# Performance work log

Hardware: AMD Instinct MI355X
Metric: run time of the kernel (lower is better)

The kernel has to match this reference:

```python
import jax, jax.numpy as jnp
import numpy as np

GAMMA = 0.5
K = 3
SKIP_THRESHOLD = 1.0


def setup_inputs() -> dict:
    key = jax.random.key(0)
    ks = jax.random.split(key, 11)
    in_dim, out_dim, mem_len = 1024, 128, 131072
    inp = {
        "x": jax.random.normal(ks[0], (1, in_dim), jnp.float32),
        "mean": jax.random.normal(ks[1], (in_dim,), jnp.float32),
        "std": jax.random.uniform(ks[2], (in_dim,), jnp.float32, 0.5, 1.5),
        "memory": jax.random.normal(ks[3], (mem_len, out_dim), jnp.float32),
        "mem_data": jax.random.normal(ks[4], (mem_len, in_dim), jnp.float32),
        "W_enc": jax.random.normal(ks[5], (in_dim, out_dim), jnp.float32) * 0.02,
        "b_enc": jnp.zeros((out_dim,), jnp.float32),
        "W_dec": jax.random.normal(ks[6], (out_dim, in_dim), jnp.float32) * 0.02,
        "b_dec": jnp.zeros((in_dim,), jnp.float32),
        "win_mean": jnp.zeros((), jnp.float32),   # WindowLoss running mean
        "win_std": jnp.ones((), jnp.float32),     # WindowLoss sample std (1 if population_std==0)
    }
    return inp


def reference(x, mean, std, memory, mem_data, W_enc, b_enc, W_dec, b_dec, win_mean, win_std):
    # normalize: new = (x - mean) / std, zero where std == 0
    new = jnp.where(std == 0, 0.0, (x - mean) / std)            # [1, in_dim]
    # encoder: Linear + Tanh
    enc = jnp.tanh(new @ W_enc + b_enc)                          # [1, out_dim]
    # window_loss: decoder reconstruction MSE, gated by ndtr of z-scored loss
    rec = enc @ W_dec + b_dec                                    # [1, in_dim]
    mse = jnp.mean((rec - new) ** 2)                             # scalar
    prob = jax.scipy.special.ndtr((mse - win_mean) / win_std)    # torch uses loss.item() -> constant
    win_loss = (SKIP_THRESHOLD - prob) / SKIP_THRESHOLD * mse
    # L1-distance top-k (smallest) against the memory bank
    dist = jnp.sum(jnp.abs(memory - enc), axis=1)                # [mem_len]
    neg_d, idx = jax.lax.top_k(-dist, K)
    distances = -neg_d                                           # [K] smallest distances
    expw = GAMMA ** jnp.arange(K, dtype=jnp.float32)
    loss_values = jnp.sum(distances * expw) / jnp.sum(expw)
    # conditional FIFO scatter update at the nearest index
    cond = loss_values <= win_loss
    i0 = idx[0]
    new_memory = jnp.where(cond, memory.at[i0].set(enc[0]), memory)
    new_mem_data = jnp.where(cond, mem_data.at[i0].set(x[0]), mem_data)
    loss_combined = win_loss + loss_values
    return loss_combined, new_memory, new_mem_data
```

## Files before the change

kernel.cpp:

```cpp
#include <hip/hip_runtime.h>
#include <math.h>
#include <float.h>

#define IN_DIM   1024
#define OUT_DIM  128
#define MEM_LEN  131072
#define COPY_GRID 1024
#define DIST_BLOCKS 2048

#define NA_FLOATS  ((long long)MEM_LEN * OUT_DIM)
#define NB_FLOATS  ((long long)MEM_LEN * IN_DIM)
#define N_TOTAL    (NA_FLOATS + NB_FLOATS)
#define NFRAMES    (N_TOTAL / 1024)
#define NPAIRS     (NFRAMES / 2)
#define FRAME_MEM  16384

typedef float f4 __attribute__((ext_vector_type(4)));

__device__ __forceinline__ void ins3(float v, int i,
    float& v0, int& i0, float& v1, int& i1, float& v2, int& i2) {
  if (v < v0 || (v == v0 && i < i0)) {
    v2 = v1; i2 = i1; v1 = v0; i1 = i0; v0 = v; i0 = i;
  } else if (v < v1 || (v == v1 && i < i1)) {
    v2 = v1; i2 = i1; v1 = v; i1 = i;
  } else if (v < v2 || (v == v2 && i < i2)) {
    v2 = v; i2 = i;
  }
}

__global__ __launch_bounds__(256) void k1a_enc(
    const float* __restrict__ x, const float* __restrict__ mean,
    const float* __restrict__ stdv, const float* __restrict__ W_enc,
    const float* __restrict__ b_enc, float* __restrict__ ws_enc) {
  const int o = blockIdx.x;
  const int t = threadIdx.x;
  float partial = 0.0f;
  #pragma unroll
  for (int j = 0; j < 4; ++j) {
    const int k = t + 256 * j;
    const float sd = stdv[k];
    const float nv = (sd == 0.0f) ? 0.0f : (x[k] - mean[k]) / sd;
    partial += nv * W_enc[k * OUT_DIM + o];
  }
  for (int off = 32; off; off >>= 1) partial += __shfl_xor(partial, off, 64);
  __shared__ float s[4];
  if ((t & 63) == 0) s[t >> 6] = partial;
  __syncthreads();
  if (t == 0) ws_enc[o] = tanhf(s[0] + s[1] + s[2] + s[3] + b_enc[o]);
}

__global__ __launch_bounds__(128) void k1b_dec(
    const float* __restrict__ x, const float* __restrict__ mean,
    const float* __restrict__ stdv, const float* __restrict__ W_dec,
    const float* __restrict__ b_dec, const float* __restrict__ ws_enc,
    float* __restrict__ ws_sse) {
  const int t = threadIdx.x;
  const int o = blockIdx.x * 128 + t;
  __shared__ float s_enc[OUT_DIM];
  s_enc[t] = ws_enc[t];
  __syncthreads();
  float r = b_dec[o];
  #pragma unroll 8
  for (int k = 0; k < OUT_DIM; ++k) r += s_enc[k] * W_dec[k * IN_DIM + o];
  const float sd = stdv[o];
  const float nv = (sd == 0.0f) ? 0.0f : (x[o] - mean[o]) / sd;
  const float diff = r - nv;
  float sq = diff * diff;
  for (int off = 32; off; off >>= 1) sq += __shfl_xor(sq, off, 64);
  __shared__ float sr[2];
  if ((t & 63) == 0) sr[t >> 6] = sq;
  __syncthreads();
  if (t == 0) ws_sse[blockIdx.x] = sr[0] + sr[1];
}

__global__ __launch_bounds__(256) void k2_dist(
    const float* __restrict__ memory, const float* __restrict__ ws_enc,
    float* __restrict__ topv, int* __restrict__ topi) {
  const int t = threadIdx.x;
  const int lane = t & 63;
  const int wid = t >> 6;
  const int half = lane >> 5;
  const int col  = lane & 31;
  const float4 e = reinterpret_cast<const float4*>(ws_enc)[col];
  const float4* m4 = reinterpret_cast<const float4*>(memory);
  float v0 = FLT_MAX, v1 = FLT_MAX, v2 = FLT_MAX;
  int i0 = 0x7fffffff, i1 = 0x7fffffff, i2 = 0x7fffffff;
  const int r0 = (blockIdx.x * 4 + wid) * 16;
  for (int rr = 0; rr < 16; rr += 2) {
    const float4 m = m4[(size_t)(r0 + rr) * 32 + lane];
    float d = fabsf(m.x - e.x) + fabsf(m.y - e.y)
            + fabsf(m.z - e.z) + fabsf(m.w - e.w);
    d += __shfl_xor(d, 1, 64);
    d += __shfl_xor(d, 2, 64);
    d += __shfl_xor(d, 4, 64);
    d += __shfl_xor(d, 8, 64);
    d += __shfl_xor(d, 16, 64);
    ins3(d, r0 + rr + half, v0, i0, v1, i1, v2, i2);
  }
  {
    const float w0 = __shfl_xor(v0, 32, 64);
    const float w1 = __shfl_xor(v1, 32, 64);
    const float w2 = __shfl_xor(v2, 32, 64);
    const int j0 = __shfl_xor(i0, 32, 64);
    const int j1 = __shfl_xor(i1, 32, 64);
    const int j2 = __shfl_xor(i2, 32, 64);
    ins3(w0, j0, v0, i0, v1, i1, v2, i2);
    ins3(w1, j1, v0, i0, v1, i1, v2, i2);
    ins3(w2, j2, v0, i0, v1, i1, v2, i2);
  }
  __shared__ float sv[4][3];
  __shared__ int   si[4][3];
  if (lane == 0) {
    sv[wid][0] = v0; sv[wid][1] = v1; sv[wid][2] = v2;
    si[wid][0] = i0; si[wid][1] = i1; si[wid][2] = i2;
  }
  __syncthreads();
  if (t == 0) {
    for (int w = 1; w < 4; ++w)
      for (int j = 0; j < 3; ++j)
        ins3(sv[w][j], si[w][j], v0, i0, v1, i1, v2, i2);
    topv[blockIdx.x * 3 + 0] = v0; topi[blockIdx.x * 3 + 0] = i0;
    topv[blockIdx.x * 3 + 1] = v1; topi[blockIdx.x * 3 + 1] = i1;
    topv[blockIdx.x * 3 + 2] = v2; topi[blockIdx.x * 3 + 2] = i2;
  }
}

__global__ __launch_bounds__(256) void copy_all(
    const float* __restrict__ memory, const float* __restrict__ mem_data,
    float* __restrict__ out) {
  const int t = threadIdx.x;
  const int lane = t & 63;
  const int wid  = t >> 6;
  const f4* mem4 = reinterpret_cast<const f4*>(memory);
  const f4* md4  = reinterpret_cast<const f4*>(mem_data);
  f4* out4 = reinterpret_cast<f4*>(out);
  const long long wstride = (long long)gridDim.x * 4;
  for (long long P = (long long)blockIdx.x * 4 + wid; P < NPAIRS; P += wstride) {
    const long long sA = 2 * P;
    const f4* srcA = (sA < FRAME_MEM) ? (mem4 + (sA << 8))
                                      : (md4 + ((sA - FRAME_MEM) << 8));
    const f4* srcB = srcA + 256;
    float edge = 0.0f;
    if (P > 0) {
      const long long sd = (sA << 10) - 1;
      edge = (sd < NA_FLOATS) ? memory[sd] : mem_data[sd - NA_FLOATS];
    }
    const f4 a0 = srcA[lane];
    const f4 a1 = srcA[lane + 64];
    const f4 a2 = srcA[lane + 128];
    const f4 a3 = srcA[lane + 192];
    const f4 b0 = srcB[lane];
    const f4 b1 = srcB[lane + 64];
    const f4 b2 = srcB[lane + 128];
    const f4 b3 = srcB[lane + 192];
    float p0 = __shfl_up(a0.w, 1, 64);
    float p1 = __shfl_up(a1.w, 1, 64);
    float p2 = __shfl_up(a2.w, 1, 64);
    float p3 = __shfl_up(a3.w, 1, 64);
    float q0 = __shfl_up(b0.w, 1, 64);
    float q1 = __shfl_up(b1.w, 1, 64);
    float q2 = __shfl_up(b2.w, 1, 64);
    float q3 = __shfl_up(b3.w, 1, 64);
    const float tA1 = __shfl(a0.w, 63, 64);
    const float tA2 = __shfl(a1.w, 63, 64);
    const float tA3 = __shfl(a2.w, 63, 64);
    const float tB0 = __shfl(a3.w, 63, 64);
    const float tB1 = __shfl(b0.w, 63, 64);
    const float tB2 = __shfl(b1.w, 63, 64);
    const float tB3 = __shfl(b2.w, 63, 64);
    if (lane == 0) {
      p0 = edge; p1 = tA1; p2 = tA2; p3 = tA3;
      q0 = tB0;  q1 = tB1; q2 = tB2; q3 = tB3;
    }
    f4* oA = out4 + (sA << 8);
    f4 w;
    w.x = p0; w.y = a0.x; w.z = a0.y; w.w = a0.z;
    __builtin_nontemporal_store(w, oA + lane);
    w.x = p1; w.y = a1.x; w.z = a1.y; w.w = a1.z;
    __builtin_nontemporal_store(w, oA + lane + 64);
    w.x = p2; w.y = a2.x; w.z = a2.y; w.w = a2.z;
    __builtin_nontemporal_store(w, oA + lane + 128);
    w.x = p3; w.y = a3.x; w.z = a3.y; w.w = a3.z;
    __builtin_nontemporal_store(w, oA + lane + 192);
    f4* oB = oA + 256;
    w.x = q0; w.y = b0.x; w.z = b0.y; w.w = b0.z;
    __builtin_nontemporal_store(w, oB + lane);
    w.x = q1; w.y = b1.x; w.z = b1.y; w.w = b1.z;
    __builtin_nontemporal_store(w, oB + lane + 64);
    w.x = q2; w.y = b2.x; w.z = b2.y; w.w = b2.z;
    __builtin_nontemporal_store(w, oB + lane + 128);
    w.x = q3; w.y = b3.x; w.z = b3.y; w.w = b3.z;
    __builtin_nontemporal_store(w, oB + lane + 192);
  }
  if (blockIdx.x == 0 && t == 0)
    out[N_TOTAL] = mem_data[NB_FLOATS - 1];
}

__global__ __launch_bounds__(1024) void k3_topk_update(
    const float* __restrict__ topv, const int* __restrict__ topi,
    const float* __restrict__ ws_sse, const float* __restrict__ win_mean,
    const float* __restrict__ win_std, const float* __restrict__ ws_enc,
    const float* __restrict__ x, float* __restrict__ out_loss,
    float* __restrict__ out_mem, float* __restrict__ out_md) {
  const int t = threadIdx.x;
  const int n = DIST_BLOCKS * 3;
  float v0 = FLT_MAX, v1 = FLT_MAX, v2 = FLT_MAX;
  int i0 = 0x7fffffff, i1 = 0x7fffffff, i2 = 0x7fffffff;
  for (int j = t; j < n; j += 1024) ins3(topv[j], topi[j], v0, i0, v1, i1, v2, i2);
  for (int off = 32; off; off >>= 1) {
    const float ov0 = __shfl_xor(v0, off, 64);
    const float ov1 = __shfl_xor(v1, off, 64);
    const float ov2 = __shfl_xor(v2, off, 64);
    const int oi0 = __shfl_xor(i0, off, 64);
    const int oi1 = __shfl_xor(i1, off, 64);
    const int oi2 = __shfl_xor(i2, off, 64);
    ins3(ov0, oi0, v0, i0, v1, i1, v2, i2);
    ins3(ov1, oi1, v0, i0, v1, i1, v2, i2);
    ins3(ov2, oi2, v0, i0, v1, i1, v2, i2);
  }
  __shared__ float sv[16][3];
  __shared__ int   si[16][3];
  __shared__ int s_i0, s_cond;
  const int lane = t & 63, wid = t >> 6;
  if (lane == 0) {
    sv[wid][0] = v0; sv[wid][1] = v1; sv[wid][2] = v2;
    si[wid][0] = i0; si[wid][1] = i1; si[wid][2] = i2;
  }
  __syncthreads();
  if (t == 0) {
    for (int w = 1; w < 16; ++w)
      for (int j = 0; j < 3; ++j)
        ins3(sv[w][j], si[w][j], v0, i0, v1, i1, v2, i2);
    float sse = 0.0f;
    #pragma unroll
    for (int b = 0; b < 8; ++b) sse += ws_sse[b];
    const float mse = sse / (float)IN_DIM;
    const float z = (mse - win_mean[0]) / win_std[0];
    const float prob = 0.5f * erfcf(-z * 0.70710678118654752440f);
    const float wl = (1.0f - prob) * mse;
    const float loss_values = (v0 + 0.5f * v1 + 0.25f * v2) / 1.75f;
    out_loss[0] = wl + loss_values;
    s_i0 = i0;
    s_cond = (loss_values <= wl) ? 1 : 0;
  }
  __syncthreads();
  if (s_cond) {
    if (t < OUT_DIM) out_mem[(size_t)s_i0 * OUT_DIM + t] = ws_enc[t];
    out_md[(size_t)s_i0 * IN_DIM + t] = x[t];
  }
}

extern "C" void kernel_launch(void* const* d_in, const int* in_sizes, int n_in,
                              void* d_out, int out_size, void* d_ws, size_t ws_size,
                              hipStream_t stream) {
  const float* x        = (const float*)d_in[0];
  const float* mean     = (const float*)d_in[1];
  const float* stdv     = (const float*)d_in[2];
  const float* memory   = (const float*)d_in[3];
  const float* mem_data = (const float*)d_in[4];
  const float* W_enc    = (const float*)d_in[5];
  const float* b_enc    = (const float*)d_in[6];
  const float* W_dec    = (const float*)d_in[7];
  const float* b_dec    = (const float*)d_in[8];
  const float* win_mean = (const float*)d_in[9];
  const float* win_std  = (const float*)d_in[10];

  float* out      = (float*)d_out;
  float* out_loss = out;
  float* out_mem  = out + 1;
  float* out_md   = out + 1 + (size_t)MEM_LEN * OUT_DIM;

  float* ws        = (float*)d_ws;
  float* ws_enc    = ws;
  float* ws_sse    = ws + 128;
  float* ws_topv   = ws + 256;
  int*   ws_topi   = (int*)(ws + 256 + DIST_BLOCKS * 3);

  k1a_enc<<<OUT_DIM, 256, 0, stream>>>(x, mean, stdv, W_enc, b_enc, ws_enc);
  k2_dist<<<DIST_BLOCKS, 256, 0, stream>>>(memory, ws_enc, ws_topv, ws_topi);
  k1b_dec<<<8, 128, 0, stream>>>(x, mean, stdv, W_dec, b_dec, ws_enc, ws_sse);
  copy_all<<<COPY_GRID, 256, 0, stream>>>(memory, mem_data, out);
  k3_topk_update<<<1, 1024, 0, stream>>>(ws_topv, ws_topi, ws_sse, win_mean,
                                         win_std, ws_enc, x,
                                         out_loss, out_mem, out_md);
}
```

Before: 321.9 us.

## Fuse L1 distance top-k computation into the memory copy kernel

Merges the distance/top-k kernel into the copy kernel, so the memory bank rows loaded for the shifted output copy are reused to compute L1 distances. This avoids a second full read of the memory bank and one kernel launch. Per-block candidate count is halved to match the new grid. Stores are changed from nontemporal to regular, which may alter cache behavior on the large streaming write.

After: 308.1 us. -4.3%, faster.

```diff
diff --git a/kernel.cpp b/kernel.cpp
--- a/kernel.cpp
+++ b/kernel.cpp
@@ -5,8 +5,8 @@
 #define IN_DIM   1024
 #define OUT_DIM  128
 #define MEM_LEN  131072
-#define COPY_GRID 1024
-#define DIST_BLOCKS 2048
+#define GRID_F   1024
+#define CAND_BLOCKS 1024
 
 #define NA_FLOATS  ((long long)MEM_LEN * OUT_DIM)
 #define NB_FLOATS  ((long long)MEM_LEN * IN_DIM)
@@ -14,8 +14,7 @@
 #define NFRAMES    (N_TOTAL / 1024)
 #define NPAIRS     (NFRAMES / 2)
 #define FRAME_MEM  16384
-
-typedef float f4 __attribute__((ext_vector_type(4)));
+#define NPAIRS_MEM 8192
 
 __device__ __forceinline__ void ins3(float v, int i,
     float& v0, int& i0, float& v1, int& i1, float& v2, int& i2) {
@@ -73,86 +72,55 @@
   if (t == 0) ws_sse[blockIdx.x] = sr[0] + sr[1];
 }
 
-__global__ __launch_bounds__(256) void k2_dist(
-    const float* __restrict__ memory, const float* __restrict__ ws_enc,
+__global__ __launch_bounds__(256) void fused_copy_dist(
+    const float* __restrict__ memory, const float* __restrict__ mem_data,
+    const float* __restrict__ ws_enc, float* __restrict__ out,
     float* __restrict__ topv, int* __restrict__ topi) {
   const int t = threadIdx.x;
   const int lane = t & 63;
-  const int wid = t >> 6;
-  const int half = lane >> 5;
-  const int col  = lane & 31;
-  const float4 e = reinterpret_cast<const float4*>(ws_enc)[col];
-  const float4* m4 = reinterpret_cast<const float4*>(memory);
+  const int wid  = t >> 6;
+  const float4* mem4 = reinterpret_cast<const float4*>(memory);
+  const float4* md4  = reinterpret_cast<const float4*>(mem_data);
+  float4* out4 = reinterpret_cast<float4*>(out);
+  const float4 e = reinterpret_cast<const float4*>(ws_enc)[lane & 31];
   float v0 = FLT_MAX, v1 = FLT_MAX, v2 = FLT_MAX;
   int i0 = 0x7fffffff, i1 = 0x7fffffff, i2 = 0x7fffffff;
-  const int r0 = (blockIdx.x * 4 + wid) * 16;
-  for (int rr = 0; rr < 16; rr += 2) {
-    const float4 m = m4[(size_t)(r0 + rr) * 32 + lane];
-    float d = fabsf(m.x - e.x) + fabsf(m.y - e.y)
-            + fabsf(m.z - e.z) + fabsf(m.w - e.w);
-    d += __shfl_xor(d, 1, 64);
-    d += __shfl_xor(d, 2, 64);
-    d += __shfl_xor(d, 4, 64);
-    d += __shfl_xor(d, 8, 64);
-    d += __shfl_xor(d, 16, 64);
-    ins3(d, r0 + rr + half, v0, i0, v1, i1, v2, i2);
-  }
-  {
-    const float w0 = __shfl_xor(v0, 32, 64);
-    const float w1 = __shfl_xor(v1, 32, 64);
-    const float w2 = __shfl_xor(v2, 32, 64);
-    const int j0 = __shfl_xor(i0, 32, 64);
-    const int j1 = __shfl_xor(i1, 32, 64);
-    const int j2 = __shfl_xor(i2, 32, 64);
-    ins3(w0, j0, v0, i0, v1, i1, v2, i2);
-    ins3(w1, j1, v0, i0, v1, i1, v2, i2);
-    ins3(w2, j2, v0, i0, v1, i1, v2, i2);
-  }
-  __shared__ float sv[4][3];
-  __shared__ int   si[4][3];
-  if (lane == 0) {
-    sv[wid][0] = v0; sv[wid][1] = v1; sv[wid][2] = v2;
-    si[wid][0] = i0; si[wid][1] = i1; si[wid][2] = i2;
-  }
-  __syncthreads();
-  if (t == 0) {
-    for (int w = 1; w < 4; ++w)
-      for (int j = 0; j < 3; ++j)
-        ins3(sv[w][j], si[w][j], v0, i0, v1, i1, v2, i2);
-    topv[blockIdx.x * 3 + 0] = v0; topi[blockIdx.x * 3 + 0] = i0;
-    topv[blockIdx.x * 3 + 1] = v1; topi[blockIdx.x * 3 + 1] = i1;
-    topv[blockIdx.x * 3 + 2] = v2; topi[blockIdx.x * 3 + 2] = i2;
-  }
-}
-
-__global__ __launch_bounds__(256) void copy_all(
-    const float* __restrict__ memory, const float* __restrict__ mem_data,
-    float* __restrict__ out) {
-  const int t = threadIdx.x;
-  const int lane = t & 63;
-  const int wid  = t >> 6;
-  const f4* mem4 = reinterpret_cast<const f4*>(memory);
-  const f4* md4  = reinterpret_cast<const f4*>(mem_data);
-  f4* out4 = reinterpret_cast<f4*>(out);
-  const long long wstride = (long long)gridDim.x * 4;
+  const long long wstride = (long long)GRID_F * 4;
   for (long long P = (long long)blockIdx.x * 4 + wid; P < NPAIRS; P += wstride) {
     const long long sA = 2 * P;
-    const f4* srcA = (sA < FRAME_MEM) ? (mem4 + (sA << 8))
-                                      : (md4 + ((sA - FRAME_MEM) << 8));
-    const f4* srcB = srcA + 256;
+    const float4* srcA = (sA < FRAME_MEM) ? (mem4 + (sA << 8))
+                                          : (md4 + ((sA - FRAME_MEM) << 8));
+    const float4* srcB = srcA + 256;
     float edge = 0.0f;
     if (P > 0) {
       const long long sd = (sA << 10) - 1;
       edge = (sd < NA_FLOATS) ? memory[sd] : mem_data[sd - NA_FLOATS];
     }
-    const f4 a0 = srcA[lane];
-    const f4 a1 = srcA[lane + 64];
-    const f4 a2 = srcA[lane + 128];
-    const f4 a3 = srcA[lane + 192];
-    const f4 b0 = srcB[lane];
-    const f4 b1 = srcB[lane + 64];
-    const f4 b2 = srcB[lane + 128];
-    const f4 b3 = srcB[lane + 192];
+    const float4 a0 = srcA[lane];
+    const float4 a1 = srcA[lane + 64];
+    const float4 a2 = srcA[lane + 128];
+    const float4 a3 = srcA[lane + 192];
+    const float4 b0 = srcB[lane];
+    const float4 b1 = srcB[lane + 64];
+    const float4 b2 = srcB[lane + 128];
+    const float4 b3 = srcB[lane + 192];
+    if (P < NPAIRS_MEM) {
+      const int rbase = (int)(16 * P) + (lane >> 5);
+#define DIST_Q(V, Q)                                                         \
+      {                                                                      \
+        float d = fabsf(V.x - e.x) + fabsf(V.y - e.y)                        \
+                + fabsf(V.z - e.z) + fabsf(V.w - e.w);                       \
+        d += __shfl_xor(d, 1, 64);                                           \
+        d += __shfl_xor(d, 2, 64);                                           \
+        d += __shfl_xor(d, 4, 64);                                           \
+        d += __shfl_xor(d, 8, 64);                                           \
+        d += __shfl_xor(d, 16, 64);                                          \
+        ins3(d, rbase + (Q), v0, i0, v1, i1, v2, i2);                        \
+      }
+      DIST_Q(a0, 0)  DIST_Q(a1, 2)  DIST_Q(a2, 4)  DIST_Q(a3, 6)
+      DIST_Q(b0, 8)  DIST_Q(b1, 10) DIST_Q(b2, 12) DIST_Q(b3, 14)
+#undef DIST_Q
+    }
     float p0 = __shfl_up(a0.w, 1, 64);
     float p1 = __shfl_up(a1.w, 1, 64);
     float p2 = __shfl_up(a2.w, 1, 64);
@@ -172,28 +140,33 @@
       p0 = edge; p1 = tA1; p2 = tA2; p3 = tA3;
       q0 = tB0;  q1 = tB1; q2 = tB2; q3 = tB3;
     }
-    f4* oA = out4 + (sA << 8);
-    f4 w;
-    w.x = p0; w.y = a0.x; w.z = a0.y; w.w = a0.z;
-    __builtin_nontemporal_store(w, oA + lane);
-    w.x = p1; w.y = a1.x; w.z = a1.y; w.w = a1.z;
-    __builtin_nontemporal_store(w, oA + lane + 64);
-    w.x = p2; w.y = a2.x; w.z = a2.y; w.w = a2.z;
-    __builtin_nontemporal_store(w, oA + lane + 128);
-    w.x = p3; w.y = a3.x; w.z = a3.y; w.w = a3.z;
-    __builtin_nontemporal_store(w, oA + lane + 192);
-    f4* oB = oA + 256;
-    w.x = q0; w.y = b0.x; w.z = b0.y; w.w = b0.z;
-    __builtin_nontemporal_store(w, oB + lane);
-    w.x = q1; w.y = b1.x; w.z = b1.y; w.w = b1.z;
-    __builtin_nontemporal_store(w, oB + lane + 64);
-    w.x = q2; w.y = b2.x; w.z = b2.y; w.w = b2.z;
-    __builtin_nontemporal_store(w, oB + lane + 128);
-    w.x = q3; w.y = b3.x; w.z = b3.y; w.w = b3.z;
-    __builtin_nontemporal_store(w, oB + lane + 192);
-  }
-  if (blockIdx.x == 0 && t == 0)
-    out[N_TOTAL] = mem_data[NB_FLOATS - 1];
+    float4* oA = out4 + (sA << 8);
+    oA[lane]       = make_float4(p0, a0.x, a0.y, a0.z);
+    oA[lane + 64]  = make_float4(p1, a1.x, a1.y, a1.z);
+    oA[lane + 128] = make_float4(p2, a2.x, a2.y, a2.z);
+    oA[lane + 192] = make_float4(p3, a3.x, a3.y, a3.z);
+    float4* oB = oA + 256;
+    oB[lane]       = make_float4(q0, b0.x, b0.y, b0.z);
+    oB[lane + 64]  = make_float4(q1, b1.x, b1.y, b1.z);
+    oB[lane + 128] = make_float4(q2, b2.x, b2.y, b2.z);
+    oB[lane + 192] = make_float4(q3, b3.x, b3.y, b3.z);
+  }
+  __shared__ float sv[4][3];
+  __shared__ int   si[4][3];
+  if (lane == 0) {
+    sv[wid][0] = v0; sv[wid][1] = v1; sv[wid][2] = v2;
+    si[wid][0] = i0; si[wid][1] = i1; si[wid][2] = i2;
+  }
+  __syncthreads();
+  if (t == 0) {
+    for (int w = 1; w < 4; ++w)
+      for (int j = 0; j < 3; ++j)
+        ins3(sv[w][j], si[w][j], v0, i0, v1, i1, v2, i2);
+    topv[blockIdx.x * 3 + 0] = v0; topi[blockIdx.x * 3 + 0] = i0;
+    topv[blockIdx.x * 3 + 1] = v1; topi[blockIdx.x * 3 + 1] = i1;
+    topv[blockIdx.x * 3 + 2] = v2; topi[blockIdx.x * 3 + 2] = i2;
+    if (blockIdx.x == 0) out[N_TOTAL] = mem_data[NB_FLOATS - 1];
+  }
 }
 
 __global__ __launch_bounds__(1024) void k3_topk_update(
@@ -203,7 +176,7 @@
     const float* __restrict__ x, float* __restrict__ out_loss,
     float* __restrict__ out_mem, float* __restrict__ out_md) {
   const int t = threadIdx.x;
-  const int n = DIST_BLOCKS * 3;
+  const int n = CAND_BLOCKS * 3;
   float v0 = FLT_MAX, v1 = FLT_MAX, v2 = FLT_MAX;
   int i0 = 0x7fffffff, i1 = 0x7fffffff, i2 = 0x7fffffff;
   for (int j = t; j < n; j += 1024) ins3(topv[j], topi[j], v0, i0, v1, i1, v2, i2);
@@ -274,12 +247,12 @@
   float* ws_enc    = ws;
   float* ws_sse    = ws + 128;
   float* ws_topv   = ws + 256;
-  int*   ws_topi   = (int*)(ws + 256 + DIST_BLOCKS * 3);
+  int*   ws_topi   = (int*)(ws + 256 + CAND_BLOCKS * 3);
 
   k1a_enc<<<OUT_DIM, 256, 0, stream>>>(x, mean, stdv, W_enc, b_enc, ws_enc);
-  k2_dist<<<DIST_BLOCKS, 256, 0, stream>>>(memory, ws_enc, ws_topv, ws_topi);
   k1b_dec<<<8, 128, 0, stream>>>(x, mean, stdv, W_dec, b_dec, ws_enc, ws_sse);
-  copy_all<<<COPY_GRID, 256, 0, stream>>>(memory, mem_data, out);
+  fused_copy_dist<<<GRID_F, 256, 0, stream>>>(memory, mem_data, ws_enc, out,
+                                              ws_topv, ws_topi);
   k3_topk_update<<<1, 1024, 0, stream>>>(ws_topv, ws_topi, ws_sse, win_mean,
                                          win_std, ws_enc, x,
                                          out_loss, out_mem, out_md);
```
